# Kernel tuning notes

Measured on AMD Instinct MI355X. Metric: run time of the kernel, lower is better.

## Reference

```python
import math
import jax, jax.numpy as jnp
import numpy as np

L, H, W_SIZE, EPS = 4, 4, 64, 1e-5


def _sinusoidal_pe(T, D):
    pos = np.arange(T, dtype=np.float32)[:, None]
    div = np.exp(np.arange(0, D, 2, dtype=np.float32) * -(math.log(10000.0) / D))
    pe = np.zeros((T, D), dtype=np.float32)
    pe[:, 0::2] = np.sin(pos * div)
    pe[:, 1::2] = np.cos(pos * div)
    return jnp.asarray(pe)


def _layernorm(x, g, b):
    mu = jnp.mean(x, axis=-1, keepdims=True)
    var = jnp.mean(jnp.square(x - mu), axis=-1, keepdims=True)
    return (x - mu) * jax.lax.rsqrt(var + EPS) * g + b


def setup_inputs() -> dict:
    key = jax.random.key(0)
    B, T, D, F = 4, 2048, 256, 1024
    ks = jax.random.split(key, 8)
    s = 0.02
    return {
        "tokens": jax.random.normal(ks[0], (B, T, D), jnp.float32),
        "Wqkv": jax.random.normal(ks[1], (L, 3 * D, D), jnp.float32) * s,
        "bqkv": jnp.zeros((L, 3 * D), jnp.float32),
        "Wo": jax.random.normal(ks[2], (L, D, D), jnp.float32) * s,
        "bo": jnp.zeros((L, D), jnp.float32),
        "W1": jax.random.normal(ks[3], (L, F, D), jnp.float32) * s,
        "b1": jnp.zeros((L, F), jnp.float32),
        "W2": jax.random.normal(ks[4], (L, D, F), jnp.float32) * s,
        "b2": jnp.zeros((L, D), jnp.float32),
        "ln1_g": jnp.ones((L, D), jnp.float32),
        "ln1_b": jnp.zeros((L, D), jnp.float32),
        "ln2_g": jnp.ones((L, D), jnp.float32),
        "ln2_b": jnp.zeros((L, D), jnp.float32),
        "lnf_g": jnp.ones((D,), jnp.float32),
        "lnf_b": jnp.zeros((D,), jnp.float32),
    }


def reference(tokens, Wqkv, bqkv, Wo, bo, W1, b1, W2, b2,
              ln1_g, ln1_b, ln2_g, ln2_b, lnf_g, lnf_b):
    B, T, D = tokens.shape
    hd = D // H
    x = tokens + _sinusoidal_pe(T, D)[None]  # (B,T,D)

    # sliding-window causal mask: i attends to max(0, i-W+1)..i
    idx = jnp.arange(T)
    i, j = idx[:, None], idx[None, :]
    allowed = (j <= i) & (j >= i - W_SIZE + 1)
    bias = jnp.where(allowed, 0.0, -1e9).astype(jnp.float32)  # (T,T)

    def step(x, p):
        Wqkv, bqkv, Wo, bo, W1, b1, W2, b2, g1, be1, g2, be2 = p
        x2 = _layernorm(x, g1, be1)
        qkv = x2 @ Wqkv.T + bqkv                      # (B,T,3D)
        q, k, v = jnp.split(qkv, 3, axis=-1)
        q = q.reshape(B, T, H, hd)
        k = k.reshape(B, T, H, hd)
        v = v.reshape(B, T, H, hd)
        scores = jnp.einsum("bthd,bshd->bhts", q, k) / math.sqrt(hd)
        attn = jax.nn.softmax(scores + bias, axis=-1)
        o = jnp.einsum("bhts,bshd->bthd", attn, v).reshape(B, T, D)
        x = x + o @ Wo.T + bo
        x3 = _layernorm(x, g2, be2)
        h = jax.nn.gelu(x3 @ W1.T + b1, approximate=False)
        x = x + h @ W2.T + b2
        return x, None

    x, _ = jax.lax.scan(step, x, (Wqkv, bqkv, Wo, bo, W1, b1, W2, b2,
                                  ln1_g, ln1_b, ln2_g, ln2_b))
    return _layernorm(x, lnf_g, lnf_b)
```

## Files before the change

kernel.cpp:

```cpp
#include <hip/hip_runtime.h>
#include <hip/hip_bf16.h>
#include <math.h>

#define BB 4
#define TT 2048
#define DD 256
#define FF 1024
#define NL 4

typedef __bf16 bf16x8 __attribute__((ext_vector_type(8)));
typedef float f32x4 __attribute__((ext_vector_type(4)));

__global__ __launch_bounds__(256) void f2b_kernel(const float4* __restrict__ in,
                                                  ushort4* __restrict__ out) {
  int i = blockIdx.x * 256 + threadIdx.x;
  float4 v = in[i];
  ushort4 o;
  o.x = __hip_bfloat16_raw(__float2bfloat16(v.x)).x;
  o.y = __hip_bfloat16_raw(__float2bfloat16(v.y)).x;
  o.z = __hip_bfloat16_raw(__float2bfloat16(v.z)).x;
  o.w = __hip_bfloat16_raw(__float2bfloat16(v.w)).x;
  out[i] = o;
}

__global__ __launch_bounds__(256) void pe_kernel(const float* __restrict__ tokens,
                                                 float* __restrict__ x) {
  int idx = blockIdx.x * 256 + threadIdx.x;
  int d = idx & (DD - 1);
  int t = (idx / DD) & (TT - 1);
  int i2 = d & ~1;
  float freq = expf((float)i2 * -(9.210340371976184f / 256.f));
  float ang = (float)t * freq;
  float pe = (d & 1) ? cosf(ang) : sinf(ang);
  x[idx] = tokens[idx] + pe;
}

template <int OBF>
__global__ __launch_bounds__(256) void ln_kernel(const float* __restrict__ x,
                                                 const float* __restrict__ g,
                                                 const float* __restrict__ b,
                                                 void* __restrict__ yv) {
  int row = blockIdx.x * 4 + (threadIdx.x >> 6);
  int lane = threadIdx.x & 63;
  const float* xr = x + (size_t)row * DD;
  float v[4];
  float s = 0.f;
#pragma unroll
  for (int i = 0; i < 4; ++i) { v[i] = xr[lane + 64 * i]; s += v[i]; }
#pragma unroll
  for (int off = 32; off; off >>= 1) s += __shfl_xor(s, off, 64);
  float mu = s * (1.f / DD);
  float vs = 0.f;
#pragma unroll
  for (int i = 0; i < 4; ++i) { float dd = v[i] - mu; vs = fmaf(dd, dd, vs); }
#pragma unroll
  for (int off = 32; off; off >>= 1) vs += __shfl_xor(vs, off, 64);
  float rr = rsqrtf(vs * (1.f / DD) + 1e-5f);
#pragma unroll
  for (int i = 0; i < 4; ++i) {
    int d = lane + 64 * i;
    float y = (v[i] - mu) * rr * g[d] + b[d];
    if (OBF) ((__hip_bfloat16*)yv)[(size_t)row * DD + d] = __float2bfloat16(y);
    else ((float*)yv)[(size_t)row * DD + d] = y;
  }
}

template <int MW, int NW, int ACT, int RES, int OBF>
__global__ __launch_bounds__(256) void mgemm_kernel(
    const __hip_bfloat16* __restrict__ A, const __hip_bfloat16* __restrict__ B,
    const float* __restrict__ bias, const float* __restrict__ res,
    void* __restrict__ Cout, int M, int N, int K) {
  constexpr int BM = 32 * MW, BN = 32 * NW;
  constexpr int ROWS = BM + BN;
  __shared__ __align__(16) __hip_bfloat16 sm[ROWS * 32];
  const int tid = threadIdx.x;
  const int wave = tid >> 6, lane = tid & 63;
  const int m0 = blockIdx.y * BM, n0 = blockIdx.x * BN;
  const int wm = (wave >> 1) * (16 * MW), wn = (wave & 1) * (16 * NW);
  const int qk = lane >> 4;
  const int lr = lane & 15;
  const int srow = lane >> 2;
  const int scol = (lane & 3) * 8;

  f32x4 acc[MW][NW] = {};

  for (int kt = 0; kt < K; kt += 32) {
    __syncthreads();
#pragma unroll
    for (int i = 0; i < ROWS / 64; ++i) {
      int inst = i * 4 + wave;
      int r = inst * 16 + srow;
      const __hip_bfloat16* g =
          (r < BM) ? (A + (size_t)(m0 + r) * K + kt + scol)
                   : (B + (size_t)(n0 + (r - BM)) * K + kt + scol);
      __builtin_amdgcn_global_load_lds(
          (const __attribute__((address_space(1))) unsigned int*)g,
          (__attribute__((address_space(3))) unsigned int*)(sm + inst * 512),
          16, 0, 0);
    }
    __syncthreads();
    bf16x8 af[MW], bfr[NW];
#pragma unroll
    for (int mi = 0; mi < MW; ++mi)
      af[mi] = *(const bf16x8*)(sm + (wm + mi * 16 + lr) * 32 + qk * 8);
#pragma unroll
    for (int ni = 0; ni < NW; ++ni)
      bfr[ni] = *(const bf16x8*)(sm + (BM + wn + ni * 16 + lr) * 32 + qk * 8);
#pragma unroll
    for (int mi = 0; mi < MW; ++mi)
#pragma unroll
      for (int ni = 0; ni < NW; ++ni)
        acc[mi][ni] = __builtin_amdgcn_mfma_f32_16x16x32_bf16(
            af[mi], bfr[ni], acc[mi][ni], 0, 0, 0);
  }

#pragma unroll
  for (int mi = 0; mi < MW; ++mi) {
#pragma unroll
    for (int ni = 0; ni < NW; ++ni) {
      int col = n0 + wn + ni * 16 + lr;
      float bv = bias[col];
#pragma unroll
      for (int r = 0; r < 4; ++r) {
        int row = m0 + wm + mi * 16 + qk * 4 + r;
        float v = acc[mi][ni][r] + bv;
        if (ACT == 1) v = 0.5f * v * (1.f + erff(v * 0.70710678118654752f));
        if (RES) v += res[(size_t)row * N + col];
        if (OBF) ((__hip_bfloat16*)Cout)[(size_t)row * N + col] = __float2bfloat16(v);
        else ((float*)Cout)[(size_t)row * N + col] = v;
      }
    }
  }
}

__global__ __launch_bounds__(256) void attn_kernel(const __hip_bfloat16* __restrict__ qkv,
                                                   __hip_bfloat16* __restrict__ o) {
  __shared__ __align__(16) __hip_bfloat16 Ks[128][72];
  __shared__ __align__(16) __hip_bfloat16 Vt[64][136];
  __shared__ __align__(16) __hip_bfloat16 Ps[4][16][136];
  const int bh = blockIdx.y;
  const int b = bh >> 2, h = bh & 3;
  const int t0 = blockIdx.x * 64;
  const int sbase = t0 - 63;
  const int tid = threadIdx.x;

  const __hip_bfloat16* kb = qkv + (size_t)(b * TT) * 768 + 256 + h * 64;
  const __hip_bfloat16* vb = kb + 256;
  union U8 { uint4 u; __hip_bfloat16 hx[8]; };
#pragma unroll
  for (int it = 0; it < 4; ++it) {
    int f = tid + it * 256;
    int si = f >> 3;
    int c8 = f & 7;
    int s = sbase + si;
    U8 kr, vr;
    kr.u = make_uint4(0, 0, 0, 0); vr.u = make_uint4(0, 0, 0, 0);
    if (s >= 0 && s < TT) {
      kr.u = *(const uint4*)&kb[(size_t)s * 768 + 8 * c8];
      vr.u = *(const uint4*)&vb[(size_t)s * 768 + 8 * c8];
    }
    *(uint4*)&Ks[si][c8 * 8] = kr.u;
#pragma unroll
    for (int j = 0; j < 8; ++j) Vt[c8 * 8 + j][si] = vr.hx[j];
  }
  __syncthreads();

  const int wave = tid >> 6, lane = tid & 63;
  const int quad = lane >> 4, lr = lane & 15;

  const __hip_bfloat16* qrow = qkv + (size_t)(b * TT + t0 + wave * 16 + lr) * 768 + h * 64;
  bf16x8 qa0 = *(const bf16x8*)(qrow + quad * 8);
  bf16x8 qa1 = *(const bf16x8*)(qrow + 32 + quad * 8);
  f32x4 sc[8];
#pragma unroll
  for (int c = 0; c < 8; ++c) {
    f32x4 a = {};
    bf16x8 kf0 = *(const bf16x8*)&Ks[c * 16 + lr][quad * 8];
    a = __builtin_amdgcn_mfma_f32_16x16x32_bf16(qa0, kf0, a, 0, 0, 0);
    bf16x8 kf1 = *(const bf16x8*)&Ks[c * 16 + lr][32 + quad * 8];
    a = __builtin_amdgcn_mfma_f32_16x16x32_bf16(qa1, kf1, a, 0, 0, 0);
    sc[c] = a;
  }

#pragma unroll
  for (int reg = 0; reg < 4; ++reg) {
    int dt = wave * 16 + quad * 4 + reg;
    float pv[8];
    float mx = -1e30f;
#pragma unroll
    for (int c = 0; c < 8; ++c) {
      int si = c * 16 + lr;
      float v = sc[c][reg] * 0.125f;
      bool ok = (si >= dt) && (si <= dt + 63) && (sbase + si >= 0);
      v = ok ? v : -1e30f;
      pv[c] = v;
      mx = fmaxf(mx, v);
    }
#pragma unroll
    for (int off = 8; off; off >>= 1) mx = fmaxf(mx, __shfl_xor(mx, off, 64));
    float l = 0.f;
#pragma unroll
    for (int c = 0; c < 8; ++c) { float e = __expf(pv[c] - mx); pv[c] = e; l += e; }
#pragma unroll
    for (int off = 8; off; off >>= 1) l += __shfl_xor(l, off, 64);
    float rinv = 1.f / l;
#pragma unroll
    for (int c = 0; c < 8; ++c)
      Ps[wave][quad * 4 + reg][c * 16 + lr] = __float2bfloat16(pv[c] * rinv);
  }

  __hip_bfloat16* obase = o + (size_t)(b * TT) * DD + h * 64;
#pragma unroll
  for (int ct = 0; ct < 4; ++ct) {
    f32x4 acc = {};
#pragma unroll
    for (int kk = 0; kk < 4; ++kk) {
      bf16x8 pa = *(const bf16x8*)&Ps[wave][lr][kk * 32 + quad * 8];
      bf16x8 vf = *(const bf16x8*)&Vt[ct * 16 + lr][kk * 32 + quad * 8];
      acc = __builtin_amdgcn_mfma_f32_16x16x32_bf16(pa, vf, acc, 0, 0, 0);
    }
#pragma unroll
    for (int reg = 0; reg < 4; ++reg) {
      int t = t0 + wave * 16 + quad * 4 + reg;
      obase[(size_t)t * DD + ct * 16 + lr] = __float2bfloat16(acc[reg]);
    }
  }
}

extern "C" void kernel_launch(void* const* d_in, const int* in_sizes, int n_in,
                              void* d_out, int out_size, void* d_ws, size_t ws_size,
                              hipStream_t stream) {
  const float* tokens = (const float*)d_in[0];
  const float* Wqkv = (const float*)d_in[1];
  const float* bqkv = (const float*)d_in[2];
  const float* Wo   = (const float*)d_in[3];
  const float* bo   = (const float*)d_in[4];
  const float* W1   = (const float*)d_in[5];
  const float* b1   = (const float*)d_in[6];
  const float* W2   = (const float*)d_in[7];
  const float* b2   = (const float*)d_in[8];
  const float* ln1g = (const float*)d_in[9];
  const float* ln1b = (const float*)d_in[10];
  const float* ln2g = (const float*)d_in[11];
  const float* ln2b = (const float*)d_in[12];
  const float* lnfg = (const float*)d_in[13];
  const float* lnfb = (const float*)d_in[14];
  float* out = (float*)d_out;

  const int M = BB * TT;
  const int ND = M * DD;

  float* x = (float*)d_ws;
  __hip_bfloat16* sb  = (__hip_bfloat16*)(x + ND);
  __hip_bfloat16* big = sb + (size_t)M * DD;
  __hip_bfloat16* wqb = big + (size_t)M * FF;
  __hip_bfloat16* wob = wqb + (size_t)NL * 3 * DD * DD;
  __hip_bfloat16* w1b = wob + (size_t)NL * DD * DD;
  __hip_bfloat16* w2b = w1b + (size_t)NL * FF * DD;

  f2b_kernel<<<(NL * 3 * DD * DD) / 1024, 256, 0, stream>>>((const float4*)Wqkv, (ushort4*)wqb);
  f2b_kernel<<<(NL * DD * DD) / 1024, 256, 0, stream>>>((const float4*)Wo, (ushort4*)wob);
  f2b_kernel<<<(NL * FF * DD) / 1024, 256, 0, stream>>>((const float4*)W1, (ushort4*)w1b);
  f2b_kernel<<<(NL * DD * FF) / 1024, 256, 0, stream>>>((const float4*)W2, (ushort4*)w2b);

  pe_kernel<<<ND / 256, 256, 0, stream>>>(tokens, x);

  for (int l = 0; l < NL; ++l) {
    ln_kernel<1><<<M / 4, 256, 0, stream>>>(x, ln1g + l * DD, ln1b + l * DD, sb);
    mgemm_kernel<4, 4, 0, 0, 1><<<dim3(768 / 128, M / 128), 256, 0, stream>>>(
        sb, wqb + (size_t)l * 768 * DD, bqkv + l * 768, nullptr, big, M, 768, DD);
    attn_kernel<<<dim3(TT / 64, BB * 4), 256, 0, stream>>>(big, sb);
    mgemm_kernel<2, 4, 0, 1, 0><<<dim3(DD / 128, M / 64), 256, 0, stream>>>(
        sb, wob + (size_t)l * DD * DD, bo + l * DD, x, x, M, DD, DD);
    ln_kernel<1><<<M / 4, 256, 0, stream>>>(x, ln2g + l * DD, ln2b + l * DD, sb);
    mgemm_kernel<4, 4, 1, 0, 1><<<dim3(FF / 128, M / 128), 256, 0, stream>>>(
        sb, w1b + (size_t)l * FF * DD, b1 + l * FF, nullptr, big, M, FF, DD);
    mgemm_kernel<2, 4, 0, 1, 0><<<dim3(DD / 128, M / 64), 256, 0, stream>>>(
        big, w2b + (size_t)l * DD * FF, b2 + l * DD, x, x, M, DD, FF);
  }

  ln_kernel<0><<<M / 4, 256, 0, stream>>>(x, lnfg, lnfb, out);
}
```

Measured before the change: 421.1 us.

## Fuse LayerNorm into residual GEMM epilogues, merge weight casts and PE, swizzle V

```diff
diff --git a/kernel.cpp b/kernel.cpp
--- a/kernel.cpp
+++ b/kernel.cpp
@@ -11,42 +11,48 @@
 typedef __bf16 bf16x8 __attribute__((ext_vector_type(8)));
 typedef float f32x4 __attribute__((ext_vector_type(4)));
 
-__global__ __launch_bounds__(256) void f2b_kernel(const float4* __restrict__ in,
-                                                  ushort4* __restrict__ out) {
-  int i = blockIdx.x * 256 + threadIdx.x;
-  float4 v = in[i];
+__global__ __launch_bounds__(256) void f2b_all_kernel(const float4* __restrict__ wq,
+                                                      const float4* __restrict__ wo,
+                                                      const float4* __restrict__ w1,
+                                                      const float4* __restrict__ w2,
+                                                      ushort4* __restrict__ dst) {
+  int gi = blockIdx.x * 256 + threadIdx.x;
+  const float4* src;
+  int off;
+  if (gi < 196608)      { src = wq; off = gi; }
+  else if (gi < 262144) { src = wo; off = gi - 196608; }
+  else if (gi < 524288) { src = w1; off = gi - 262144; }
+  else                  { src = w2; off = gi - 524288; }
+  float4 v = src[off];
   ushort4 o;
   o.x = __hip_bfloat16_raw(__float2bfloat16(v.x)).x;
   o.y = __hip_bfloat16_raw(__float2bfloat16(v.y)).x;
   o.z = __hip_bfloat16_raw(__float2bfloat16(v.z)).x;
   o.w = __hip_bfloat16_raw(__float2bfloat16(v.w)).x;
-  out[i] = o;
-}
-
-__global__ __launch_bounds__(256) void pe_kernel(const float* __restrict__ tokens,
-                                                 float* __restrict__ x) {
-  int idx = blockIdx.x * 256 + threadIdx.x;
-  int d = idx & (DD - 1);
-  int t = (idx / DD) & (TT - 1);
-  int i2 = d & ~1;
-  float freq = expf((float)i2 * -(9.210340371976184f / 256.f));
-  float ang = (float)t * freq;
-  float pe = (d & 1) ? cosf(ang) : sinf(ang);
-  x[idx] = tokens[idx] + pe;
-}
-
-template <int OBF>
-__global__ __launch_bounds__(256) void ln_kernel(const float* __restrict__ x,
-                                                 const float* __restrict__ g,
-                                                 const float* __restrict__ b,
-                                                 void* __restrict__ yv) {
+  dst[gi] = o;
+}
+
+__global__ __launch_bounds__(256) void pe_ln_kernel(const float* __restrict__ tokens,
+                                                    const float* __restrict__ g,
+                                                    const float* __restrict__ b,
+                                                    float* __restrict__ x,
+                                                    __hip_bfloat16* __restrict__ sb) {
   int row = blockIdx.x * 4 + (threadIdx.x >> 6);
   int lane = threadIdx.x & 63;
-  const float* xr = x + (size_t)row * DD;
+  int t = row & (TT - 1);
+  const float* xr = tokens + (size_t)row * DD;
   float v[4];
   float s = 0.f;
 #pragma unroll
-  for (int i = 0; i < 4; ++i) { v[i] = xr[lane + 64 * i]; s += v[i]; }
+  for (int i = 0; i < 4; ++i) {
+    int d = lane + 64 * i;
+    int i2 = d & ~1;
+    float freq = expf((float)i2 * -(9.210340371976184f / 256.f));
+    float ang = (float)t * freq;
+    float pe = (d & 1) ? cosf(ang) : sinf(ang);
+    v[i] = xr[d] + pe;
+    s += v[i];
+  }
 #pragma unroll
   for (int off = 32; off; off >>= 1) s += __shfl_xor(s, off, 64);
   float mu = s * (1.f / DD);
@@ -59,19 +65,19 @@
 #pragma unroll
   for (int i = 0; i < 4; ++i) {
     int d = lane + 64 * i;
-    float y = (v[i] - mu) * rr * g[d] + b[d];
-    if (OBF) ((__hip_bfloat16*)yv)[(size_t)row * DD + d] = __float2bfloat16(y);
-    else ((float*)yv)[(size_t)row * DD + d] = y;
-  }
-}
-
-template <int MW, int NW, int ACT, int RES, int OBF>
+    x[(size_t)row * DD + d] = v[i];
+    sb[(size_t)row * DD + d] = __float2bfloat16((v[i] - mu) * rr * g[d] + b[d]);
+  }
+}
+
+template <int MW, int NW, int ACT>
 __global__ __launch_bounds__(256) void mgemm_kernel(
     const __hip_bfloat16* __restrict__ A, const __hip_bfloat16* __restrict__ B,
-    const float* __restrict__ bias, const float* __restrict__ res,
-    void* __restrict__ Cout, int M, int N, int K) {
+    const float* __restrict__ bias, __hip_bfloat16* __restrict__ Cout,
+    int M, int N, int K) {
   constexpr int BM = 32 * MW, BN = 32 * NW;
   constexpr int ROWS = BM + BN;
+  constexpr int NINST = ROWS / 16;
   __shared__ __align__(16) __hip_bfloat16 sm[ROWS * 32];
   const int tid = threadIdx.x;
   const int wave = tid >> 6, lane = tid & 63;
@@ -87,16 +93,18 @@
   for (int kt = 0; kt < K; kt += 32) {
     __syncthreads();
 #pragma unroll
-    for (int i = 0; i < ROWS / 64; ++i) {
+    for (int i = 0; i < (NINST + 3) / 4; ++i) {
       int inst = i * 4 + wave;
-      int r = inst * 16 + srow;
-      const __hip_bfloat16* g =
-          (r < BM) ? (A + (size_t)(m0 + r) * K + kt + scol)
-                   : (B + (size_t)(n0 + (r - BM)) * K + kt + scol);
-      __builtin_amdgcn_global_load_lds(
-          (const __attribute__((address_space(1))) unsigned int*)g,
-          (__attribute__((address_space(3))) unsigned int*)(sm + inst * 512),
-          16, 0, 0);
+      if (inst < NINST) {
+        int r = inst * 16 + srow;
+        const __hip_bfloat16* g =
+            (r < BM) ? (A + (size_t)(m0 + r) * K + kt + scol)
+                     : (B + (size_t)(n0 + (r - BM)) * K + kt + scol);
+        __builtin_amdgcn_global_load_lds(
+            (const __attribute__((address_space(1))) unsigned int*)g,
+            (__attribute__((address_space(3))) unsigned int*)(sm + inst * 512),
+            16, 0, 0);
+      }
     }
     __syncthreads();
     bf16x8 af[MW], bfr[NW];
@@ -125,9 +133,105 @@
         int row = m0 + wm + mi * 16 + qk * 4 + r;
         float v = acc[mi][ni][r] + bv;
         if (ACT == 1) v = 0.5f * v * (1.f + erff(v * 0.70710678118654752f));
-        if (RES) v += res[(size_t)row * N + col];
-        if (OBF) ((__hip_bfloat16*)Cout)[(size_t)row * N + col] = __float2bfloat16(v);
-        else ((float*)Cout)[(size_t)row * N + col] = v;
+        Cout[(size_t)row * N + col] = __float2bfloat16(v);
+      }
+    }
+  }
+}
+
+template <int FIN>
+__global__ __launch_bounds__(256) void mgemm_ln_kernel(
+    const __hip_bfloat16* __restrict__ A, const __hip_bfloat16* __restrict__ B,
+    const float* __restrict__ bias, const float* __restrict__ res,
+    const float* __restrict__ g, const float* __restrict__ bb,
+    float* __restrict__ xout, void* __restrict__ yout, int K) {
+  constexpr int NINST = 17;
+  __shared__ __align__(16) __hip_bfloat16 sm[(16 + 256) * 32];
+  __shared__ float red1[4][16], red2[4][16];
+  const int tid = threadIdx.x;
+  const int wave = tid >> 6, lane = tid & 63;
+  const int quad = lane >> 4, lr = lane & 15;
+  const int m0 = blockIdx.x * 16;
+  const int srow = lane >> 2, scol = (lane & 3) * 8;
+
+  f32x4 acc[4] = {};
+
+  for (int kt = 0; kt < K; kt += 32) {
+    __syncthreads();
+#pragma unroll
+    for (int i = 0; i < 5; ++i) {
+      int inst = i * 4 + wave;
+      if (inst < NINST) {
+        int r = inst * 16 + srow;
+        const __hip_bfloat16* gp =
+            (r < 16) ? (A + (size_t)(m0 + r) * K + kt + scol)
+                     : (B + (size_t)(r - 16) * K + kt + scol);
+        __builtin_amdgcn_global_load_lds(
+            (const __attribute__((address_space(1))) unsigned int*)gp,
+            (__attribute__((address_space(3))) unsigned int*)(sm + inst * 512),
+            16, 0, 0);
+      }
+    }
+    __syncthreads();
+    bf16x8 af = *(const bf16x8*)(sm + lr * 32 + quad * 8);
+    bf16x8 bfr[4];
+#pragma unroll
+    for (int ni = 0; ni < 4; ++ni)
+      bfr[ni] = *(const bf16x8*)(sm + (16 + wave * 64 + ni * 16 + lr) * 32 + quad * 8);
+#pragma unroll
+    for (int ni = 0; ni < 4; ++ni)
+      acc[ni] = __builtin_amdgcn_mfma_f32_16x16x32_bf16(af, bfr[ni], acc[ni], 0, 0, 0);
+  }
+
+  float v[4][4];
+  float s1[4] = {}, s2[4] = {};
+#pragma unroll
+  for (int ni = 0; ni < 4; ++ni) {
+    int col = wave * 64 + ni * 16 + lr;
+    float bv = bias[col];
+#pragma unroll
+    for (int r = 0; r < 4; ++r) {
+      int row = m0 + quad * 4 + r;
+      float val = acc[ni][r] + bv + res[(size_t)row * DD + col];
+      v[ni][r] = val;
+      s1[r] += val;
+      s2[r] = fmaf(val, val, s2[r]);
+    }
+  }
+#pragma unroll
+  for (int r = 0; r < 4; ++r) {
+#pragma unroll
+    for (int off = 8; off; off >>= 1) {
+      s1[r] += __shfl_xor(s1[r], off, 64);
+      s2[r] += __shfl_xor(s2[r], off, 64);
+    }
+  }
+  if (lr == 0) {
+#pragma unroll
+    for (int r = 0; r < 4; ++r) {
+      red1[wave][quad * 4 + r] = s1[r];
+      red2[wave][quad * 4 + r] = s2[r];
+    }
+  }
+  __syncthreads();
+#pragma unroll
+  for (int r = 0; r < 4; ++r) {
+    int rl = quad * 4 + r;
+    float ssum = red1[0][rl] + red1[1][rl] + red1[2][rl] + red1[3][rl];
+    float qsum = red2[0][rl] + red2[1][rl] + red2[2][rl] + red2[3][rl];
+    float mu = ssum * (1.f / DD);
+    float var = qsum * (1.f / DD) - mu * mu;
+    float rr = rsqrtf(var + 1e-5f);
+    int row = m0 + rl;
+#pragma unroll
+    for (int ni = 0; ni < 4; ++ni) {
+      int col = wave * 64 + ni * 16 + lr;
+      float y = (v[ni][r] - mu) * rr * g[col] + bb[col];
+      if (FIN) {
+        ((float*)yout)[(size_t)row * DD + col] = y;
+      } else {
+        ((__hip_bfloat16*)yout)[(size_t)row * DD + col] = __float2bfloat16(y);
+        xout[(size_t)row * DD + col] = v[ni][r];
       }
     }
   }
@@ -136,7 +240,7 @@
 __global__ __launch_bounds__(256) void attn_kernel(const __hip_bfloat16* __restrict__ qkv,
                                                    __hip_bfloat16* __restrict__ o) {
   __shared__ __align__(16) __hip_bfloat16 Ks[128][72];
-  __shared__ __align__(16) __hip_bfloat16 Vt[64][136];
+  __shared__ __align__(16) __hip_bfloat16 Vt[64 * 136];
   __shared__ __align__(16) __hip_bfloat16 Ps[4][16][136];
   const int bh = blockIdx.y;
   const int b = bh >> 2, h = bh & 3;
@@ -160,8 +264,9 @@
       vr.u = *(const uint4*)&vb[(size_t)s * 768 + 8 * c8];
     }
     *(uint4*)&Ks[si][c8 * 8] = kr.u;
-#pragma unroll
-    for (int j = 0; j < 8; ++j) Vt[c8 * 8 + j][si] = vr.hx[j];
+    int pc = (si >> 3) ^ c8;
+#pragma unroll
+    for (int j = 0; j < 8; ++j) Vt[(c8 * 8 + j) * 136 + pc * 8 + (si & 7)] = vr.hx[j];
   }
   __syncthreads();
 
@@ -216,7 +321,8 @@
 #pragma unroll
     for (int kk = 0; kk < 4; ++kk) {
       bf16x8 pa = *(const bf16x8*)&Ps[wave][lr][kk * 32 + quad * 8];
-      bf16x8 vf = *(const bf16x8*)&Vt[ct * 16 + lr][kk * 32 + quad * 8];
+      int dd = ct * 16 + lr;
+      bf16x8 vf = *(const bf16x8*)&Vt[dd * 136 + (((kk * 4 + quad) ^ (dd >> 3)) * 8)];
       acc = __builtin_amdgcn_mfma_f32_16x16x32_bf16(pa, vf, acc, 0, 0, 0);
     }
 #pragma unroll
@@ -258,26 +364,29 @@
   __hip_bfloat16* w1b = wob + (size_t)NL * DD * DD;
   __hip_bfloat16* w2b = w1b + (size_t)NL * FF * DD;
 
-  f2b_kernel<<<(NL * 3 * DD * DD) / 1024, 256, 0, stream>>>((const float4*)Wqkv, (ushort4*)wqb);
-  f2b_kernel<<<(NL * DD * DD) / 1024, 256, 0, stream>>>((const float4*)Wo, (ushort4*)wob);
-  f2b_kernel<<<(NL * FF * DD) / 1024, 256, 0, stream>>>((const float4*)W1, (ushort4*)w1b);
-  f2b_kernel<<<(NL * DD * FF) / 1024, 256, 0, stream>>>((const float4*)W2, (ushort4*)w2b);
-
-  pe_kernel<<<ND / 256, 256, 0, stream>>>(tokens, x);
+  f2b_all_kernel<<<3072, 256, 0, stream>>>(
+      (const float4*)Wqkv, (const float4*)Wo, (const float4*)W1,
+      (const float4*)W2, (ushort4*)wqb);
+
+  pe_ln_kernel<<<M / 4, 256, 0, stream>>>(tokens, ln1g, ln1b, x, sb);
 
   for (int l = 0; l < NL; ++l) {
-    ln_kernel<1><<<M / 4, 256, 0, stream>>>(x, ln1g + l * DD, ln1b + l * DD, sb);
-    mgemm_kernel<4, 4, 0, 0, 1><<<dim3(768 / 128, M / 128), 256, 0, stream>>>(
-        sb, wqb + (size_t)l * 768 * DD, bqkv + l * 768, nullptr, big, M, 768, DD);
+    mgemm_kernel<4, 3, 0><<<dim3(768 / 96, M / 128), 256, 0, stream>>>(
+        sb, wqb + (size_t)l * 768 * DD, bqkv + l * 768, big, M, 768, DD);
     attn_kernel<<<dim3(TT / 64, BB * 4), 256, 0, stream>>>(big, sb);
-    mgemm_kernel<2, 4, 0, 1, 0><<<dim3(DD / 128, M / 64), 256, 0, stream>>>(
-        sb, wob + (size_t)l * DD * DD, bo + l * DD, x, x, M, DD, DD);
-    ln_kernel<1><<<M / 4, 256, 0, stream>>>(x, ln2g + l * DD, ln2b + l * DD, sb);
-    mgemm_kernel<4, 4, 1, 0, 1><<<dim3(FF / 128, M / 128), 256, 0, stream>>>(
-        sb, w1b + (size_t)l * FF * DD, b1 + l * FF, nullptr, big, M, FF, DD);
-    mgemm_kernel<2, 4, 0, 1, 0><<<dim3(DD / 128, M / 64), 256, 0, stream>>>(
-        big, w2b + (size_t)l * DD * FF, b2 + l * DD, x, x, M, DD, FF);
-  }
-
-  ln_kernel<0><<<M / 4, 256, 0, stream>>>(x, lnfg, lnfb, out);
-}
+    mgemm_ln_kernel<0><<<M / 16, 256, 0, stream>>>(
+        sb, wob + (size_t)l * DD * DD, bo + l * DD, x,
+        ln2g + l * DD, ln2b + l * DD, x, sb, DD);
+    mgemm_kernel<4, 4, 1><<<dim3(FF / 128, M / 128), 256, 0, stream>>>(
+        sb, w1b + (size_t)l * FF * DD, b1 + l * FF, big, M, FF, DD);
+    if (l < NL - 1) {
+      mgemm_ln_kernel<0><<<M / 16, 256, 0, stream>>>(
+          big, w2b + (size_t)l * DD * FF, b2 + l * DD, x,
+          ln1g + (l + 1) * DD, ln1b + (l + 1) * DD, x, sb, FF);
+    } else {
+      mgemm_ln_kernel<1><<<M / 16, 256, 0, stream>>>(
+          big, w2b + (size_t)l * DD * FF, b2 + l * DD, x,
+          lnfg, lnfb, nullptr, out, FF);
+    }
+  }
+}
```

Result: faster. 388.9 us (-7.7%).
